# Optimization experiments

Measured on AMD Instinct MI355X. Metric: run time of the kernel, lower is better.

The kernel has to match this reference:

```python
import jax, jax.numpy as jnp
import numpy as np

B, NAT, K, F, L = 16, 256, 24, 128, 4
EPS = 0.01  # action / displacement step scale


def _gather(a, idx):
    # a: [B, n, ...], idx: [B, n, k] -> [B, n, k, ...]
    return jax.vmap(lambda ab, ib: ab[ib])(a, idx)


def _knn_idx(x, cell, k):
    # periodic minimum-image kNN within each structure
    frac = x[:, None, :, :] - x[:, :, None, :]          # [B,i,j,3] = x_j - x_i
    frac = frac - jnp.round(frac)
    cart = jnp.einsum('bijd,bde->bije', frac, cell)
    dist = jnp.linalg.norm(cart, axis=-1)
    dist = dist + jnp.eye(x.shape[1], dtype=x.dtype) * 1e6  # exclude self
    _, idx = jax.lax.top_k(-dist, k)
    return idx


def _edge_vectors(x, cell, idx):
    xj = _gather(x, idx)                                # [B,n,k,3]
    frac = xj - x[:, :, None, :]
    frac = frac - jnp.round(frac)
    vec = jnp.einsum('bnkd,bde->bnke', frac, cell)
    dist = jnp.linalg.norm(vec, axis=-1)
    return vec, dist


def _mpnn(h, idx, dist, W1, b1, W2, b2):
    hj = _gather(h, idx)                                # [B,n,k,F]
    feat = jnp.concatenate([hj, dist[..., None]], axis=-1)
    m = jax.nn.silu(jnp.einsum('bnkf,fg->bnkg', feat, W1) + b1)
    return h + jax.nn.silu(m.sum(axis=2) @ W2 + b2)


def _forward(cell, x, z, emb, mW1, mb1, mW2, mb2, uW1, ub1, uW2, ub2, act_we, actpos_we):
    I = jnp.eye(3, dtype=x.dtype)
    Bc = cell.shape[0]
    cell0 = jnp.broadcast_to(I, (Bc, 3, 3))            # actions_init overrides input cell
    x = jnp.mod(x, 1.0)
    idx = _knn_idx(x, cell0, K)
    vec, dist = _edge_vectors(x, cell0, idx)
    u = vec / (dist[..., None] + 1e-12)
    cross = jnp.cross(u[:, :, :, None, :], u[:, :, None, :, :])  # [B,n,k,k,3]
    tri_mask = (jnp.linalg.norm(cross, axis=-1) > 1e-3).astype(x.dtype)  # filter_triplets

    h = emb[z]
    for l in range(L):
        h = _mpnn(h, idx, dist, mW1[l], mb1[l], mW2[l], mb2[l])

    action_rho = jnp.broadcast_to(I, (Bc, 3, 3))
    traj_sum = jnp.zeros_like(x)
    geo_cell = cell0
    rho_prime = action_rho
    for l in range(L):
        h = _mpnn(h, idx, dist, uW1[l], ub1[l], uW2[l], ub2[l])
        hj = _gather(h, idx)
        e_feat = h[:, :, None, :] + hj                  # [B,n,k,F]
        w_e = jnp.tanh(jnp.einsum('bnkf,f->bnk', e_feat, act_we[l]))
        w_t = w_e[:, :, :, None] * w_e[:, :, None, :] * tri_mask
        strain = jnp.einsum('bnk,bnkc,bnkd->bcd', w_e, u, u) / (NAT * K)
        tri = jnp.einsum('bnjk,bnjkc,bnjkd->bcd', w_t, cross, cross) / (NAT * K * K)
        action = jnp.eye(3, dtype=x.dtype) + EPS * (strain + tri)
        action_rho = jnp.einsum('bij,bjk->bik', action, action_rho)
        rho_prime = jnp.einsum('bij,bjk->bik', action_rho, cell0)
        # position actions
        w_p = jnp.tanh(jnp.einsum('bnkf,f->bnk', e_feat, actpos_we[l]))
        x_cart = EPS * jnp.einsum('bnk,bnkc->bnc', w_p, vec)
        x_frac = jnp.einsum('bnc,bcd->bnd', x_cart, jnp.linalg.inv(geo_cell))
        traj_sum = traj_sum + x_cart
        x = x + x_frac
        geo_cell = rho_prime
        vec, dist = _edge_vectors(x, geo_cell, idx)     # geometry.update_vectors()
        u = vec / (dist[..., None] + 1e-12)
        cross = jnp.cross(u[:, :, :, None, :], u[:, :, None, :, :])
    return traj_sum, rho_prime


def setup_inputs() -> dict:
    key = jax.random.key(0)
    ks = jax.random.split(key, 12)
    s1 = 1.0 / np.sqrt(F + 1)
    s2 = 1.0 / np.sqrt(F)
    return {
        'cell': jax.random.normal(ks[0], (B, 3, 3), jnp.float32),
        'x': jax.random.uniform(ks[1], (B, NAT, 3), jnp.float32),
        'z': jax.random.randint(ks[2], (B, NAT), 0, 100, dtype=jnp.int32),
        'struct_size': jnp.full((B,), NAT, dtype=jnp.int32),
        'emb': jax.random.normal(ks[3], (100, F), jnp.float32) * 0.1,
        'mpnn_W1': jax.random.normal(ks[4], (L, F + 1, F), jnp.float32) * s1,
        'mpnn_b1': jnp.zeros((L, F), jnp.float32),
        'mpnn_W2': jax.random.normal(ks[5], (L, F, F), jnp.float32) * s2,
        'mpnn_b2': jnp.zeros((L, F), jnp.float32),
        'upd_W1': jax.random.normal(ks[6], (L, F + 1, F), jnp.float32) * s1,
        'upd_b1': jnp.zeros((L, F), jnp.float32),
        'upd_W2': jax.random.normal(ks[7], (L, F, F), jnp.float32) * s2,
        'upd_b2': jnp.zeros((L, F), jnp.float32),
        'act_we': jax.random.normal(ks[8], (L, F), jnp.float32) * s2,
        'actpos_we': jax.random.normal(ks[9], (L, F), jnp.float32) * s2,
    }


def reference(cell, x, z, struct_size, emb, mpnn_W1, mpnn_b1, mpnn_W2, mpnn_b2, upd_W1, upd_b1, upd_W2, upd_b2, act_we, actpos_we):
    # struct_size is informational (dense uniform batch of NAT atoms per structure)
    return _forward(cell, x, z, emb, mpnn_W1, mpnn_b1, mpnn_W2, mpnn_b2,
                    upd_W1, upd_b1, upd_W2, upd_b2, act_we, actpos_we)
```

## Files before the change

kernel.cpp:

```cpp
#include <hip/hip_runtime.h>

#define NB 16
#define NATS 256
#define KNN 24
#define FD 128
#define EPSA 0.01f
#define NATOMS (NB * NATS)
#define NEDGE (NATOMS * KNN)

typedef __attribute__((ext_vector_type(8))) short short8;
typedef __attribute__((ext_vector_type(4))) float f32x4;

__device__ __forceinline__ float silu_f(float v) { return v / (1.f + __expf(-v)); }

__device__ __forceinline__ short f2b(float f) {
    union { float f; unsigned u; } v; v.f = f;
    unsigned r = v.u + 0x7FFFu + ((v.u >> 16) & 1u);
    return (short)(r >> 16);
}
__device__ __forceinline__ float b2f(short s) {
    return __uint_as_float(((unsigned)(unsigned short)s) << 16);
}
__device__ __forceinline__ short8 ldb(const short* __restrict__ W, int n, int ks, int quad) {
    return *(const short8*)&W[n * 128 + ks * 32 + quad * 8];
}

__global__ __launch_bounds__(256) void prep_kernel(
    const float* __restrict__ mW1, const float* __restrict__ mW2,
    const float* __restrict__ uW1, const float* __restrict__ uW2,
    short* __restrict__ wh, short* __restrict__ wl_)
{
    int tid = blockIdx.x * 256 + threadIdx.x;
    int m = tid >> 14;
    int e = tid & 16383;
    int n = e >> 7, k = e & 127;
    const float* src;
    int l = m & 3;
    switch (m >> 2) {
        case 0:  src = mW1 + l * 129 * 128; break;
        case 1:  src = mW2 + l * 128 * 128; break;
        case 2:  src = uW1 + l * 129 * 128; break;
        default: src = uW2 + l * 128 * 128; break;
    }
    float w = src[k * 128 + n];
    short hi = f2b(w);
    wh[tid] = hi;
    wl_[tid] = f2b(w - b2f(hi));
}

__global__ __launch_bounds__(256) void init_kernel(
    const float* __restrict__ xin, const int* __restrict__ z,
    const float* __restrict__ emb,
    const short* __restrict__ W1h, const short* __restrict__ W1l,
    float* __restrict__ x, float* __restrict__ traj,
    float* __restrict__ h, float* __restrict__ hW)
{
    __shared__ short sAH[16 * 136];
    __shared__ short sAL[16 * 136];
    const int t = threadIdx.x;
    const int atom0 = blockIdx.x * 16;
    if (t < 48) {
        int gi = atom0 * 3 + t;
        float v = xin[gi];
        x[gi] = v - floorf(v);
        traj[gi] = 0.f;
    }
    {
        const int r = t >> 4;
        const int f0 = (t & 15) * 8;
        const int a = atom0 + r;
        const float4* src = (const float4*)(emb + z[a] * FD + f0);
        float4 v0 = src[0], v1 = src[1];
        float4* dst = (float4*)(h + a * FD + f0);
        dst[0] = v0; dst[1] = v1;
        float vv[8] = {v0.x, v0.y, v0.z, v0.w, v1.x, v1.y, v1.z, v1.w};
        short8 shv, slv;
#pragma unroll
        for (int i = 0; i < 8; ++i) {
            short hi = f2b(vv[i]);
            shv[i] = hi; slv[i] = f2b(vv[i] - b2f(hi));
        }
        *(short8*)&sAH[r * 136 + f0] = shv;
        *(short8*)&sAL[r * 136 + f0] = slv;
    }
    __syncthreads();
    const int w = t >> 6, lane = t & 63, quad = lane >> 4, col = lane & 15;
    const int n0 = w * 32;
    f32x4 acc0 = {0.f, 0.f, 0.f, 0.f}, acc1 = {0.f, 0.f, 0.f, 0.f};
#pragma unroll
    for (int ks = 0; ks < 4; ++ks) {
        short8 ah = *(const short8*)&sAH[col * 136 + ks * 32 + quad * 8];
        short8 al = *(const short8*)&sAL[col * 136 + ks * 32 + quad * 8];
        short8 bh0 = ldb(W1h, n0 + col, ks, quad);
        short8 bl0 = ldb(W1l, n0 + col, ks, quad);
        short8 bh1 = ldb(W1h, n0 + 16 + col, ks, quad);
        short8 bl1 = ldb(W1l, n0 + 16 + col, ks, quad);
        acc0 = __builtin_amdgcn_mfma_f32_16x16x32_bf16(ah, bh0, acc0, 0, 0, 0);
        acc0 = __builtin_amdgcn_mfma_f32_16x16x32_bf16(ah, bl0, acc0, 0, 0, 0);
        acc0 = __builtin_amdgcn_mfma_f32_16x16x32_bf16(al, bh0, acc0, 0, 0, 0);
        acc1 = __builtin_amdgcn_mfma_f32_16x16x32_bf16(ah, bh1, acc1, 0, 0, 0);
        acc1 = __builtin_amdgcn_mfma_f32_16x16x32_bf16(ah, bl1, acc1, 0, 0, 0);
        acc1 = __builtin_amdgcn_mfma_f32_16x16x32_bf16(al, bh1, acc1, 0, 0, 0);
    }
#pragma unroll
    for (int nt = 0; nt < 2; ++nt) {
        int gn = n0 + nt * 16 + col;
        f32x4 av = (nt == 0) ? acc0 : acc1;
#pragma unroll
        for (int r = 0; r < 4; ++r) {
            int row = quad * 4 + r;
            hW[(atom0 + row) * FD + gn] = av[r];
        }
    }
}

__global__ __launch_bounds__(64) void knn_kernel(const float* __restrict__ x,
    int* __restrict__ idxb, float* __restrict__ u0, float* __restrict__ dist0)
{
    const int a = blockIdx.x;
    const int b = a >> 8;
    const int lane = threadIdx.x;
    const float xi0 = x[a * 3 + 0], xi1 = x[a * 3 + 1], xi2 = x[a * 3 + 2];
    unsigned long long key[4];
#pragma unroll
    for (int tt = 0; tt < 4; ++tt) {
        int jg = b * NATS + lane + tt * 64;
        float d0 = x[jg * 3 + 0] - xi0; d0 -= rintf(d0);
        float d1 = x[jg * 3 + 1] - xi1; d1 -= rintf(d1);
        float d2 = x[jg * 3 + 2] - xi2; d2 -= rintf(d2);
        float dd = sqrtf(d0 * d0 + d1 * d1 + d2 * d2);
        if (jg == a) dd += 1e6f;
        key[tt] = ((unsigned long long)__float_as_uint(dd) << 32) | (unsigned)jg;
    }
    int myj = 0;
    for (int sel = 0; sel < KNN; ++sel) {
        unsigned long long m = key[0];
        if (key[1] < m) m = key[1];
        if (key[2] < m) m = key[2];
        if (key[3] < m) m = key[3];
#pragma unroll
        for (int off = 32; off > 0; off >>= 1) {
            unsigned lo = (unsigned)__shfl_xor((int)(unsigned)(m & 0xffffffffu), off);
            unsigned hi = (unsigned)__shfl_xor((int)(unsigned)(m >> 32), off);
            unsigned long long o = ((unsigned long long)hi << 32) | lo;
            if (o < m) m = o;
        }
        int jw = (int)(m & 0xffffffffu);
        if (lane == 0) idxb[a * KNN + sel] = jw;
        if (lane == sel) myj = jw;
#pragma unroll
        for (int tt = 0; tt < 4; ++tt) if (key[tt] == m) key[tt] = ~0ull;
    }
    if (lane < KNN) {
        float f0 = x[myj * 3 + 0] - xi0; f0 -= rintf(f0);
        float f1 = x[myj * 3 + 1] - xi1; f1 -= rintf(f1);
        float f2 = x[myj * 3 + 2] - xi2; f2 -= rintf(f2);
        float dd = sqrtf(f0 * f0 + f1 * f1 + f2 * f2);
        float inv = 1.f / (dd + 1e-12f);
        int e = a * KNN + lane;
        u0[e * 3 + 0] = f0 * inv; u0[e * 3 + 1] = f1 * inv; u0[e * 3 + 2] = f2 * inv;
        dist0[e] = dd;
    }
}

__global__ __launch_bounds__(256, 2) void layer_kernel(
    const float* __restrict__ hW, const int* __restrict__ idxb,
    const float* __restrict__ dist0,
    const float* __restrict__ x, const float* __restrict__ geo, int use_geo,
    const float* __restrict__ wl, const float* __restrict__ b1,
    const short* __restrict__ W2h, const short* __restrict__ W2l,
    const float* __restrict__ b2,
    const short* __restrict__ W1nh, const short* __restrict__ W1nl,
    float* __restrict__ hWout,
    float* __restrict__ h, int write_h,
    const float* __restrict__ we_a, const float* __restrict__ we_p,
    float* __restrict__ p, float* __restrict__ q)
{
    __shared__ short sAggH[16 * 136];
    __shared__ short sAggL[16 * 136];
    __shared__ short sHnH[16 * 136];
    __shared__ short sHnL[16 * 136];
    __shared__ float sHf[8 * 136];
    __shared__ int   sIdx[8 * KNN];
    __shared__ float sDist[8 * KNN];
    const int t = threadIdx.x;
    const int atom0 = blockIdx.x * 8;
    if (t < 8 * KNN) {
        int a = atom0 + (t / KNN);
        int j = idxb[atom0 * KNN + t];
        sIdx[t] = j;
        float d;
        if (dist0 != nullptr) {
            d = dist0[atom0 * KNN + t];
        } else {
            float f0 = x[j * 3 + 0] - x[a * 3 + 0]; f0 -= rintf(f0);
            float f1 = x[j * 3 + 1] - x[a * 3 + 1]; f1 -= rintf(f1);
            float f2 = x[j * 3 + 2] - x[a * 3 + 2]; f2 -= rintf(f2);
            const float* c = geo + (a >> 8) * 9;
            float v0 = f0 * c[0] + f1 * c[3] + f2 * c[6];
            float v1 = f0 * c[1] + f1 * c[4] + f2 * c[7];
            float v2 = f0 * c[2] + f1 * c[5] + f2 * c[8];
            d = sqrtf(v0 * v0 + v1 * v1 + v2 * v2);
        }
        sDist[t] = d;
    }
    __syncthreads();
    {
        const int g = t & 127;
        const int sub = t >> 7;
        const float wlg = wl[g];
        const float b1g = b1[g];
#pragma unroll
        for (int rep = 0; rep < 4; ++rep) {
            const int a = rep * 2 + sub;
            float s = 0.f;
#pragma unroll 8
            for (int k = 0; k < KNN; ++k) {
                int j = sIdx[a * KNN + k];
                float v = hW[j * FD + g] + sDist[a * KNN + k] * wlg + b1g;
                s += silu_f(v);
            }
            short hi = f2b(s);
            sAggH[a * 136 + g] = hi;
            sAggL[a * 136 + g] = f2b(s - b2f(hi));
        }
    }
    __syncthreads();
    const int w = t >> 6, lane = t & 63, quad = lane >> 4, col = lane & 15;
    const int n0 = w * 32;
    f32x4 acc0 = {0.f, 0.f, 0.f, 0.f}, acc1 = {0.f, 0.f, 0.f, 0.f};
#pragma unroll
    for (int ks = 0; ks < 4; ++ks) {
        short8 ah = *(const short8*)&sAggH[col * 136 + ks * 32 + quad * 8];
        short8 al = *(const short8*)&sAggL[col * 136 + ks * 32 + quad * 8];
        short8 bh0 = ldb(W2h, n0 + col, ks, quad);
        short8 bl0 = ldb(W2l, n0 + col, ks, quad);
        short8 bh1 = ldb(W2h, n0 + 16 + col, ks, quad);
        short8 bl1 = ldb(W2l, n0 + 16 + col, ks, quad);
        acc0 = __builtin_amdgcn_mfma_f32_16x16x32_bf16(ah, bh0, acc0, 0, 0, 0);
        acc0 = __builtin_amdgcn_mfma_f32_16x16x32_bf16(ah, bl0, acc0, 0, 0, 0);
        acc0 = __builtin_amdgcn_mfma_f32_16x16x32_bf16(al, bh0, acc0, 0, 0, 0);
        acc1 = __builtin_amdgcn_mfma_f32_16x16x32_bf16(ah, bh1, acc1, 0, 0, 0);
        acc1 = __builtin_amdgcn_mfma_f32_16x16x32_bf16(ah, bl1, acc1, 0, 0, 0);
        acc1 = __builtin_amdgcn_mfma_f32_16x16x32_bf16(al, bh1, acc1, 0, 0, 0);
    }
#pragma unroll
    for (int nt = 0; nt < 2; ++nt) {
        int gn = n0 + nt * 16 + col;
        float bb = b2[gn];
        f32x4 av = (nt == 0) ? acc0 : acc1;
#pragma unroll
        for (int r = 0; r < 4; ++r) {
            int row = quad * 4 + r;
            if (row < 8) {
                float o = h[(atom0 + row) * FD + gn] + silu_f(av[r] + bb);
                if (write_h) h[(atom0 + row) * FD + gn] = o;
                short hi = f2b(o);
                sHnH[row * 136 + gn] = hi;
                sHnL[row * 136 + gn] = f2b(o - b2f(hi));
                sHf[row * 136 + gn] = o;
            }
        }
    }
    __syncthreads();
    if (we_a != nullptr && t < 128) {
        int a = t >> 4, gr = t & 15;
        float pp = 0.f, qq = 0.f;
#pragma unroll
        for (int i = 0; i < 8; ++i) {
            int g = gr + i * 16;
            float hv = sHf[a * 136 + g];
            pp += hv * we_a[g];
            qq += hv * we_p[g];
        }
#pragma unroll
        for (int off = 8; off >= 1; off >>= 1) {
            pp += __shfl_xor(pp, off);
            qq += __shfl_xor(qq, off);
        }
        if (gr == 0) { p[atom0 + a] = pp; q[atom0 + a] = qq; }
    }
    if (W1nh != nullptr) {
        f32x4 d0 = {0.f, 0.f, 0.f, 0.f}, d1 = {0.f, 0.f, 0.f, 0.f};
#pragma unroll
        for (int ks = 0; ks < 4; ++ks) {
            short8 ah = *(const short8*)&sHnH[col * 136 + ks * 32 + quad * 8];
            short8 al = *(const short8*)&sHnL[col * 136 + ks * 32 + quad * 8];
            short8 bh0 = ldb(W1nh, n0 + col, ks, quad);
            short8 bl0 = ldb(W1nl, n0 + col, ks, quad);
            short8 bh1 = ldb(W1nh, n0 + 16 + col, ks, quad);
            short8 bl1 = ldb(W1nl, n0 + 16 + col, ks, quad);
            d0 = __builtin_amdgcn_mfma_f32_16x16x32_bf16(ah, bh0, d0, 0, 0, 0);
            d0 = __builtin_amdgcn_mfma_f32_16x16x32_bf16(ah, bl0, d0, 0, 0, 0);
            d0 = __builtin_amdgcn_mfma_f32_16x16x32_bf16(al, bh0, d0, 0, 0, 0);
            d1 = __builtin_amdgcn_mfma_f32_16x16x32_bf16(ah, bh1, d1, 0, 0, 0);
            d1 = __builtin_amdgcn_mfma_f32_16x16x32_bf16(ah, bl1, d1, 0, 0, 0);
            d1 = __builtin_amdgcn_mfma_f32_16x16x32_bf16(al, bh1, d1, 0, 0, 0);
        }
#pragma unroll
        for (int nt = 0; nt < 2; ++nt) {
            int gn = n0 + nt * 16 + col;
            f32x4 av = (nt == 0) ? d0 : d1;
#pragma unroll
            for (int r = 0; r < 4; ++r) {
                int row = quad * 4 + r;
                if (row < 8)
                    hWout[(atom0 + row) * FD + gn] = av[r];
            }
        }
    }
}

__global__ __launch_bounds__(256) void accum_kernel(
    const float* __restrict__ p, const float* __restrict__ q,
    const int* __restrict__ idxb, const float* __restrict__ x,
    const float* __restrict__ geo, int use_geo,
    const float* __restrict__ u0b,
    float* __restrict__ part, float* __restrict__ xcart)
{
    const int blk = blockIdx.x;
    const int t = threadIdx.x;
    const int w = t >> 6;
    const int lane = t & 63;
    const int a = blk * 4 + w;
    const int b = a >> 8;
    __shared__ float swe[4][KNN], swp[4][KNN];
    __shared__ float su[4][KNN][3], su0[4][KNN][3], sv[4][KNN][3];
    __shared__ float spart[4][18];
    if (lane < KNN) {
        int e = a * KNN + lane;
        int j = idxb[e];
        swe[w][lane] = tanhf(p[a] + p[j]);
        swp[w][lane] = tanhf(q[a] + q[j]);
        float f0 = x[j * 3 + 0] - x[a * 3 + 0]; f0 -= rintf(f0);
        float f1 = x[j * 3 + 1] - x[a * 3 + 1]; f1 -= rintf(f1);
        float f2 = x[j * 3 + 2] - x[a * 3 + 2]; f2 -= rintf(f2);
        float v0 = f0, v1 = f1, v2 = f2;
        if (use_geo) {
            const float* c = geo + b * 9;
            v0 = f0 * c[0] + f1 * c[3] + f2 * c[6];
            v1 = f0 * c[1] + f1 * c[4] + f2 * c[7];
            v2 = f0 * c[2] + f1 * c[5] + f2 * c[8];
        }
        float dd = sqrtf(v0 * v0 + v1 * v1 + v2 * v2);
        float inv = 1.f / (dd + 1e-12f);
        sv[w][lane][0] = v0; sv[w][lane][1] = v1; sv[w][lane][2] = v2;
        su[w][lane][0] = v0 * inv; su[w][lane][1] = v1 * inv; su[w][lane][2] = v2 * inv;
        su0[w][lane][0] = u0b[e * 3]; su0[w][lane][1] = u0b[e * 3 + 1]; su0[w][lane][2] = u0b[e * 3 + 2];
    }
    __syncthreads();
    float r[21];
#pragma unroll
    for (int i = 0; i < 21; ++i) r[i] = 0.f;
    if (lane < KNN) {
        float wgt = swe[w][lane];
        float ux = su[w][lane][0], uy = su[w][lane][1], uz = su[w][lane][2];
        r[0] = wgt * ux * ux; r[1] = wgt * ux * uy; r[2] = wgt * ux * uz;
        r[3] = wgt * uy * ux; r[4] = wgt * uy * uy; r[5] = wgt * uy * uz;
        r[6] = wgt * uz * ux; r[7] = wgt * uz * uy; r[8] = wgt * uz * uz;
        float wp = swp[w][lane];
        r[18] = wp * sv[w][lane][0]; r[19] = wp * sv[w][lane][1]; r[20] = wp * sv[w][lane][2];
    }
#pragma unroll
    for (int tt = 0; tt < 9; ++tt) {
        int pr = lane + (tt << 6);
        int j = pr / KNN, k = pr - j * KNN;
        float c0x = su0[w][j][1] * su0[w][k][2] - su0[w][j][2] * su0[w][k][1];
        float c0y = su0[w][j][2] * su0[w][k][0] - su0[w][j][0] * su0[w][k][2];
        float c0z = su0[w][j][0] * su0[w][k][1] - su0[w][j][1] * su0[w][k][0];
        float nn2 = c0x * c0x + c0y * c0y + c0z * c0z;
        if (nn2 > 1e-6f) {
            float cx = su[w][j][1] * su[w][k][2] - su[w][j][2] * su[w][k][1];
            float cy = su[w][j][2] * su[w][k][0] - su[w][j][0] * su[w][k][2];
            float cz = su[w][j][0] * su[w][k][1] - su[w][j][1] * su[w][k][0];
            float wt = swe[w][j] * swe[w][k];
            r[9]  += wt * cx * cx; r[10] += wt * cx * cy; r[11] += wt * cx * cz;
            r[12] += wt * cy * cx; r[13] += wt * cy * cy; r[14] += wt * cy * cz;
            r[15] += wt * cz * cx; r[16] += wt * cz * cy; r[17] += wt * cz * cz;
        }
    }
#pragma unroll
    for (int off = 32; off > 0; off >>= 1)
#pragma unroll
        for (int i = 0; i < 21; ++i) r[i] += __shfl_down(r[i], off);
    if (lane == 0) {
#pragma unroll
        for (int i = 0; i < 18; ++i) spart[w][i] = r[i];
        xcart[a * 3 + 0] = EPSA * r[18];
        xcart[a * 3 + 1] = EPSA * r[19];
        xcart[a * 3 + 2] = EPSA * r[20];
    }
    __syncthreads();
    if (t < 18)
        part[blk * 18 + t] = spart[0][t] + spart[1][t] + spart[2][t] + spart[3][t];
}

__global__ __launch_bounds__(256) void rho_pos_kernel(const float* __restrict__ part,
    const float* __restrict__ xcart,
    float* __restrict__ rho, float* __restrict__ geo,
    float* __restrict__ x, float* __restrict__ traj,
    float* __restrict__ out, int first, int last)
{
    const int b = blockIdx.x;
    const int t = threadIdx.x;
    __shared__ float sIV[9];
    if (t < 64) {
        float r[18];
#pragma unroll
        for (int i = 0; i < 18; ++i) r[i] = part[(b * 64 + t) * 18 + i];
#pragma unroll
        for (int off = 32; off > 0; off >>= 1)
#pragma unroll
            for (int i = 0; i < 18; ++i) r[i] += __shfl_down(r[i], off);
        if (t == 0) {
            float A[9];
#pragma unroll
            for (int i = 0; i < 9; ++i) {
                float strain = r[i] / 6144.f;
                float tri = r[9 + i] / 147456.f;
                A[i] = ((i == 0 || i == 4 || i == 8) ? 1.f : 0.f) + EPSA * (strain + tri);
            }
            float N[9], IV[9];
            if (first) {
#pragma unroll
                for (int i = 0; i < 9; ++i) { N[i] = A[i]; IV[i] = (i == 0 || i == 4 || i == 8) ? 1.f : 0.f; }
            } else {
                float R[9], G[9];
#pragma unroll
                for (int i = 0; i < 9; ++i) { R[i] = rho[b * 9 + i]; G[i] = geo[b * 9 + i]; }
#pragma unroll
                for (int i = 0; i < 3; ++i)
#pragma unroll
                    for (int k = 0; k < 3; ++k)
                        N[i * 3 + k] = A[i * 3] * R[k] + A[i * 3 + 1] * R[3 + k] + A[i * 3 + 2] * R[6 + k];
                float det = G[0] * (G[4] * G[8] - G[5] * G[7])
                          - G[1] * (G[3] * G[8] - G[5] * G[6])
                          + G[2] * (G[3] * G[7] - G[4] * G[6]);
                float id = 1.f / det;
                IV[0] = (G[4] * G[8] - G[5] * G[7]) * id;
                IV[1] = (G[2] * G[7] - G[1] * G[8]) * id;
                IV[2] = (G[1] * G[5] - G[2] * G[4]) * id;
                IV[3] = (G[5] * G[6] - G[3] * G[8]) * id;
                IV[4] = (G[0] * G[8] - G[2] * G[6]) * id;
                IV[5] = (G[2] * G[3] - G[0] * G[5]) * id;
                IV[6] = (G[3] * G[7] - G[4] * G[6]) * id;
                IV[7] = (G[1] * G[6] - G[0] * G[7]) * id;
                IV[8] = (G[0] * G[4] - G[1] * G[3]) * id;
            }
#pragma unroll
            for (int i = 0; i < 9; ++i) {
                sIV[i] = IV[i];
                rho[b * 9 + i] = N[i];
                if (!last) geo[b * 9 + i] = N[i];
                else out[NATOMS * 3 + b * 9 + i] = N[i];
            }
        }
    }
    __syncthreads();
    for (int d = t; d < NATS * 3; d += 256) {
        int al = d / 3, dim = d - al * 3;
        int ga = b * NATS + al;
        int gi = ga * 3 + dim;
        float c0 = xcart[ga * 3 + 0], c1 = xcart[ga * 3 + 1], c2 = xcart[ga * 3 + 2];
        float tj = traj[gi] + xcart[gi];
        if (!last) {
            float xf = c0 * sIV[0 + dim] + c1 * sIV[3 + dim] + c2 * sIV[6 + dim];
            x[gi] += xf;
            traj[gi] = tj;
        } else {
            out[gi] = tj;
        }
    }
}

extern "C" void kernel_launch(void* const* d_in, const int* in_sizes, int n_in,
                              void* d_out, int out_size, void* d_ws, size_t ws_size,
                              hipStream_t stream)
{
    (void)in_sizes; (void)n_in; (void)out_size; (void)ws_size;
    const float* in_x = (const float*)d_in[1];
    const int*   z    = (const int*)d_in[2];
    const float* emb  = (const float*)d_in[4];
    const float* mW1  = (const float*)d_in[5];
    const float* mb1  = (const float*)d_in[6];
    const float* mW2  = (const float*)d_in[7];
    const float* mb2  = (const float*)d_in[8];
    const float* uW1  = (const float*)d_in[9];
    const float* ub1  = (const float*)d_in[10];
    const float* uW2  = (const float*)d_in[11];
    const float* ub2  = (const float*)d_in[12];
    const float* awe  = (const float*)d_in[13];
    const float* pwe  = (const float*)d_in[14];
    float* out = (float*)d_out;

    char* wsb = (char*)d_ws;
    size_t off = 0;
    auto carve = [&](size_t elems) {
        void* ptr = wsb + off;
        off += (elems * 4 + 255) & ~(size_t)255;
        return ptr;
    };
    float* traj  = (float*)carve(NATOMS * 3);
    float* part  = (float*)carve(1024 * 18);
    float* x     = (float*)carve(NATOMS * 3);
    float* xcart = (float*)carve(NATOMS * 3);
    float* p     = (float*)carve(NATOMS);
    float* q     = (float*)carve(NATOMS);
    float* rho   = (float*)carve(NB * 9);
    float* geo   = (float*)carve(NB * 9);
    float* u0    = (float*)carve(NEDGE * 3);
    float* dist0 = (float*)carve(NEDGE);
    float* h     = (float*)carve(NATOMS * FD);
    float* hWa   = (float*)carve(NATOMS * FD);
    float* hWb   = (float*)carve(NATOMS * FD);
    int*   idx   = (int*)carve(NEDGE);
    short* wth   = (short*)carve(16 * 16384 / 2);
    short* wtl   = (short*)carve(16 * 16384 / 2);

    auto WH = [&](int m) { return wth + m * 16384; };
    auto WL = [&](int m) { return wtl + m * 16384; };

    prep_kernel<<<1024, 256, 0, stream>>>(mW1, mW2, uW1, uW2, wth, wtl);
    init_kernel<<<256, 256, 0, stream>>>(in_x, z, emb, WH(0), WL(0), x, traj, h, hWa);
    knn_kernel<<<NATOMS, 64, 0, stream>>>(x, idx, u0, dist0);

    float* hw_in = hWa;
    float* hw_out = hWb;

    for (int l = 0; l < 4; ++l) {
        int w1n = (l < 3) ? (l + 1) : 8;
        layer_kernel<<<512, 256, 0, stream>>>(hw_in, idx, dist0, x, geo, 0,
            mW1 + l * 129 * 128 + 128 * 128, mb1 + l * 128,
            WH(4 + l), WL(4 + l), mb2 + l * 128,
            WH(w1n), WL(w1n), hw_out, h, 1,
            nullptr, nullptr, nullptr, nullptr);
        float* tmp = hw_in; hw_in = hw_out; hw_out = tmp;
    }
    for (int l = 0; l < 4; ++l) {
        const short* W1nh = (l < 3) ? WH(9 + l) : nullptr;
        const short* W1nl = (l < 3) ? WL(9 + l) : nullptr;
        const float* d0 = (l == 0) ? dist0 : nullptr;
        layer_kernel<<<512, 256, 0, stream>>>(hw_in, idx, d0, x, geo, (l > 0) ? 1 : 0,
            uW1 + l * 129 * 128 + 128 * 128, ub1 + l * 128,
            WH(12 + l), WL(12 + l), ub2 + l * 128,
            W1nh, W1nl, hw_out, h, (l < 3) ? 1 : 0,
            awe + l * 128, pwe + l * 128, p, q);
        float* tmp = hw_in; hw_in = hw_out; hw_out = tmp;
        accum_kernel<<<1024, 256, 0, stream>>>(p, q, idx, x, geo, (l > 0) ? 1 : 0,
            u0, part, xcart);
        rho_pos_kernel<<<NB, 256, 0, stream>>>(part, xcart, rho, geo, x, traj, out,
            (l == 0) ? 1 : 0, (l == 3) ? 1 : 0);
    }
}
```

Before: 339.1 us.

## Fuse kNN into first layer kernel and rho update into accum kernel

The standalone kNN kernel now runs inside the first message-passing layer kernel. Each wave computes neighbours for two atoms and writes the indices and distances straight into shared memory as well as to global buffers. The per-structure rho/position update kernel is folded into accum_kernel: a last-block-arrives atomic counter per structure (zeroed in init_kernel) lets the final block of each structure reduce the partials and update geo, x and traj. This removes five kernel launches and their inter-kernel gaps. In exchange it adds threadfence/atomic synchronisation and puts serial kNN selection work into the layer kernel.

```diff
diff --git a/kernel.cpp b/kernel.cpp
--- a/kernel.cpp
+++ b/kernel.cpp
@@ -53,12 +53,13 @@
     const float* __restrict__ emb,
     const short* __restrict__ W1h, const short* __restrict__ W1l,
     float* __restrict__ x, float* __restrict__ traj,
-    float* __restrict__ h, float* __restrict__ hW)
+    float* __restrict__ h, float* __restrict__ hW, int* __restrict__ cnt)
 {
     __shared__ short sAH[16 * 136];
     __shared__ short sAL[16 * 136];
     const int t = threadIdx.x;
     const int atom0 = blockIdx.x * 16;
+    if (blockIdx.x == 0 && t < 64) cnt[t] = 0;
     if (t < 48) {
         int gi = atom0 * 3 + t;
         float v = xin[gi];
@@ -107,66 +108,16 @@
         int gn = n0 + nt * 16 + col;
         f32x4 av = (nt == 0) ? acc0 : acc1;
 #pragma unroll
-        for (int r = 0; r < 4; ++r) {
-            int row = quad * 4 + r;
-            hW[(atom0 + row) * FD + gn] = av[r];
-        }
-    }
-}
-
-__global__ __launch_bounds__(64) void knn_kernel(const float* __restrict__ x,
-    int* __restrict__ idxb, float* __restrict__ u0, float* __restrict__ dist0)
-{
-    const int a = blockIdx.x;
-    const int b = a >> 8;
-    const int lane = threadIdx.x;
-    const float xi0 = x[a * 3 + 0], xi1 = x[a * 3 + 1], xi2 = x[a * 3 + 2];
-    unsigned long long key[4];
-#pragma unroll
-    for (int tt = 0; tt < 4; ++tt) {
-        int jg = b * NATS + lane + tt * 64;
-        float d0 = x[jg * 3 + 0] - xi0; d0 -= rintf(d0);
-        float d1 = x[jg * 3 + 1] - xi1; d1 -= rintf(d1);
-        float d2 = x[jg * 3 + 2] - xi2; d2 -= rintf(d2);
-        float dd = sqrtf(d0 * d0 + d1 * d1 + d2 * d2);
-        if (jg == a) dd += 1e6f;
-        key[tt] = ((unsigned long long)__float_as_uint(dd) << 32) | (unsigned)jg;
-    }
-    int myj = 0;
-    for (int sel = 0; sel < KNN; ++sel) {
-        unsigned long long m = key[0];
-        if (key[1] < m) m = key[1];
-        if (key[2] < m) m = key[2];
-        if (key[3] < m) m = key[3];
-#pragma unroll
-        for (int off = 32; off > 0; off >>= 1) {
-            unsigned lo = (unsigned)__shfl_xor((int)(unsigned)(m & 0xffffffffu), off);
-            unsigned hi = (unsigned)__shfl_xor((int)(unsigned)(m >> 32), off);
-            unsigned long long o = ((unsigned long long)hi << 32) | lo;
-            if (o < m) m = o;
-        }
-        int jw = (int)(m & 0xffffffffu);
-        if (lane == 0) idxb[a * KNN + sel] = jw;
-        if (lane == sel) myj = jw;
-#pragma unroll
-        for (int tt = 0; tt < 4; ++tt) if (key[tt] == m) key[tt] = ~0ull;
-    }
-    if (lane < KNN) {
-        float f0 = x[myj * 3 + 0] - xi0; f0 -= rintf(f0);
-        float f1 = x[myj * 3 + 1] - xi1; f1 -= rintf(f1);
-        float f2 = x[myj * 3 + 2] - xi2; f2 -= rintf(f2);
-        float dd = sqrtf(f0 * f0 + f1 * f1 + f2 * f2);
-        float inv = 1.f / (dd + 1e-12f);
-        int e = a * KNN + lane;
-        u0[e * 3 + 0] = f0 * inv; u0[e * 3 + 1] = f1 * inv; u0[e * 3 + 2] = f2 * inv;
-        dist0[e] = dd;
+        for (int r = 0; r < 4; ++r)
+            hW[(atom0 + quad * 4 + r) * FD + gn] = av[r];
     }
 }
 
 __global__ __launch_bounds__(256, 2) void layer_kernel(
-    const float* __restrict__ hW, const int* __restrict__ idxb,
-    const float* __restrict__ dist0,
-    const float* __restrict__ x, const float* __restrict__ geo, int use_geo,
+    const float* __restrict__ hW, int* __restrict__ idxb,
+    float* __restrict__ dist0, float* __restrict__ u0w,
+    const float* __restrict__ x, const float* __restrict__ geo,
+    int mode_knn, int use_d0, int use_geo,
     const float* __restrict__ wl, const float* __restrict__ b1,
     const short* __restrict__ W2h, const short* __restrict__ W2l,
     const float* __restrict__ b2,
@@ -185,21 +136,75 @@
     __shared__ float sDist[8 * KNN];
     const int t = threadIdx.x;
     const int atom0 = blockIdx.x * 8;
-    if (t < 8 * KNN) {
+    const int w = t >> 6, lane = t & 63, quad = lane >> 4, col = lane & 15;
+    const int n0 = w * 32;
+    if (mode_knn) {
+        for (int rep = 0; rep < 2; ++rep) {
+            const int slot = w * 2 + rep;
+            const int a = atom0 + slot;
+            const int bS = a >> 8;
+            const float xi0 = x[a * 3 + 0], xi1 = x[a * 3 + 1], xi2 = x[a * 3 + 2];
+            unsigned long long key[4];
+#pragma unroll
+            for (int tt = 0; tt < 4; ++tt) {
+                int jg = bS * NATS + lane + tt * 64;
+                float d0 = x[jg * 3 + 0] - xi0; d0 -= rintf(d0);
+                float d1 = x[jg * 3 + 1] - xi1; d1 -= rintf(d1);
+                float d2 = x[jg * 3 + 2] - xi2; d2 -= rintf(d2);
+                float dd = sqrtf(d0 * d0 + d1 * d1 + d2 * d2);
+                if (jg == a) dd += 1e6f;
+                key[tt] = ((unsigned long long)__float_as_uint(dd) << 32) | (unsigned)jg;
+            }
+            int myj = 0;
+            for (int sel = 0; sel < KNN; ++sel) {
+                unsigned long long m = key[0];
+                if (key[1] < m) m = key[1];
+                if (key[2] < m) m = key[2];
+                if (key[3] < m) m = key[3];
+#pragma unroll
+                for (int off = 32; off > 0; off >>= 1) {
+                    unsigned lo = (unsigned)__shfl_xor((int)(unsigned)(m & 0xffffffffu), off);
+                    unsigned hi = (unsigned)__shfl_xor((int)(unsigned)(m >> 32), off);
+                    unsigned long long o = ((unsigned long long)hi << 32) | lo;
+                    if (o < m) m = o;
+                }
+                int jw = (int)(m & 0xffffffffu);
+                if (lane == 0) idxb[a * KNN + sel] = jw;
+                if (lane == sel) myj = jw;
+#pragma unroll
+                for (int tt = 0; tt < 4; ++tt) if (key[tt] == m) key[tt] = ~0ull;
+            }
+            if (lane < KNN) {
+                float f0 = x[myj * 3 + 0] - xi0; f0 -= rintf(f0);
+                float f1 = x[myj * 3 + 1] - xi1; f1 -= rintf(f1);
+                float f2 = x[myj * 3 + 2] - xi2; f2 -= rintf(f2);
+                float dd = sqrtf(f0 * f0 + f1 * f1 + f2 * f2);
+                float inv = 1.f / (dd + 1e-12f);
+                int e = a * KNN + lane;
+                u0w[e * 3 + 0] = f0 * inv; u0w[e * 3 + 1] = f1 * inv; u0w[e * 3 + 2] = f2 * inv;
+                dist0[e] = dd;
+                sIdx[slot * KNN + lane] = myj;
+                sDist[slot * KNN + lane] = dd;
+            }
+        }
+    } else if (t < 8 * KNN) {
         int a = atom0 + (t / KNN);
         int j = idxb[atom0 * KNN + t];
         sIdx[t] = j;
         float d;
-        if (dist0 != nullptr) {
+        if (use_d0) {
             d = dist0[atom0 * KNN + t];
         } else {
             float f0 = x[j * 3 + 0] - x[a * 3 + 0]; f0 -= rintf(f0);
             float f1 = x[j * 3 + 1] - x[a * 3 + 1]; f1 -= rintf(f1);
             float f2 = x[j * 3 + 2] - x[a * 3 + 2]; f2 -= rintf(f2);
-            const float* c = geo + (a >> 8) * 9;
-            float v0 = f0 * c[0] + f1 * c[3] + f2 * c[6];
-            float v1 = f0 * c[1] + f1 * c[4] + f2 * c[7];
-            float v2 = f0 * c[2] + f1 * c[5] + f2 * c[8];
+            float v0 = f0, v1 = f1, v2 = f2;
+            if (use_geo) {
+                const float* c = geo + (a >> 8) * 9;
+                v0 = f0 * c[0] + f1 * c[3] + f2 * c[6];
+                v1 = f0 * c[1] + f1 * c[4] + f2 * c[7];
+                v2 = f0 * c[2] + f1 * c[5] + f2 * c[8];
+            }
             d = sqrtf(v0 * v0 + v1 * v1 + v2 * v2);
         }
         sDist[t] = d;
@@ -226,8 +231,6 @@
         }
     }
     __syncthreads();
-    const int w = t >> 6, lane = t & 63, quad = lane >> 4, col = lane & 15;
-    const int n0 = w * 32;
     f32x4 acc0 = {0.f, 0.f, 0.f, 0.f}, acc1 = {0.f, 0.f, 0.f, 0.f};
 #pragma unroll
     for (int ks = 0; ks < 4; ++ks) {
@@ -313,10 +316,12 @@
 
 __global__ __launch_bounds__(256) void accum_kernel(
     const float* __restrict__ p, const float* __restrict__ q,
-    const int* __restrict__ idxb, const float* __restrict__ x,
-    const float* __restrict__ geo, int use_geo,
+    const int* __restrict__ idxb, float* __restrict__ x,
+    float* __restrict__ geo, int use_geo,
     const float* __restrict__ u0b,
-    float* __restrict__ part, float* __restrict__ xcart)
+    float* __restrict__ part, float* __restrict__ xcart,
+    float* __restrict__ rho, float* __restrict__ traj,
+    float* __restrict__ out, int* __restrict__ cnt, int first, int last)
 {
     const int blk = blockIdx.x;
     const int t = threadIdx.x;
@@ -324,9 +329,12 @@
     const int lane = t & 63;
     const int a = blk * 4 + w;
     const int b = a >> 8;
+    const int s = blk >> 6;
     __shared__ float swe[4][KNN], swp[4][KNN];
     __shared__ float su[4][KNN][3], su0[4][KNN][3], sv[4][KNN][3];
     __shared__ float spart[4][18];
+    __shared__ int   sLast;
+    __shared__ float sIV[9];
     if (lane < KNN) {
         int e = a * KNN + lane;
         int j = idxb[e];
@@ -393,31 +401,29 @@
     __syncthreads();
     if (t < 18)
         part[blk * 18 + t] = spart[0][t] + spart[1][t] + spart[2][t] + spart[3][t];
-}
-
-__global__ __launch_bounds__(256) void rho_pos_kernel(const float* __restrict__ part,
-    const float* __restrict__ xcart,
-    float* __restrict__ rho, float* __restrict__ geo,
-    float* __restrict__ x, float* __restrict__ traj,
-    float* __restrict__ out, int first, int last)
-{
-    const int b = blockIdx.x;
-    const int t = threadIdx.x;
-    __shared__ float sIV[9];
+    __threadfence();
+    __syncthreads();
+    if (t == 0) {
+        int old = atomicAdd(&cnt[s], 1);
+        sLast = (old == 63) ? 1 : 0;
+    }
+    __syncthreads();
+    if (!sLast) return;
+    __threadfence();
     if (t < 64) {
-        float r[18];
-#pragma unroll
-        for (int i = 0; i < 18; ++i) r[i] = part[(b * 64 + t) * 18 + i];
+        float rr[18];
+#pragma unroll
+        for (int i = 0; i < 18; ++i) rr[i] = part[(s * 64 + t) * 18 + i];
 #pragma unroll
         for (int off = 32; off > 0; off >>= 1)
 #pragma unroll
-            for (int i = 0; i < 18; ++i) r[i] += __shfl_down(r[i], off);
+            for (int i = 0; i < 18; ++i) rr[i] += __shfl_down(rr[i], off);
         if (t == 0) {
             float A[9];
 #pragma unroll
             for (int i = 0; i < 9; ++i) {
-                float strain = r[i] / 6144.f;
-                float tri = r[9 + i] / 147456.f;
+                float strain = rr[i] / 6144.f;
+                float tri = rr[9 + i] / 147456.f;
                 A[i] = ((i == 0 || i == 4 || i == 8) ? 1.f : 0.f) + EPSA * (strain + tri);
             }
             float N[9], IV[9];
@@ -427,7 +433,7 @@
             } else {
                 float R[9], G[9];
 #pragma unroll
-                for (int i = 0; i < 9; ++i) { R[i] = rho[b * 9 + i]; G[i] = geo[b * 9 + i]; }
+                for (int i = 0; i < 9; ++i) { R[i] = rho[s * 9 + i]; G[i] = geo[s * 9 + i]; }
 #pragma unroll
                 for (int i = 0; i < 3; ++i)
 #pragma unroll
@@ -450,16 +456,16 @@
 #pragma unroll
             for (int i = 0; i < 9; ++i) {
                 sIV[i] = IV[i];
-                rho[b * 9 + i] = N[i];
-                if (!last) geo[b * 9 + i] = N[i];
-                else out[NATOMS * 3 + b * 9 + i] = N[i];
+                rho[s * 9 + i] = N[i];
+                if (!last) geo[s * 9 + i] = N[i];
+                else out[NATOMS * 3 + s * 9 + i] = N[i];
             }
         }
     }
     __syncthreads();
     for (int d = t; d < NATS * 3; d += 256) {
         int al = d / 3, dim = d - al * 3;
-        int ga = b * NATS + al;
+        int ga = s * NATS + al;
         int gi = ga * 3 + dim;
         float c0 = xcart[ga * 3 + 0], c1 = xcart[ga * 3 + 1], c2 = xcart[ga * 3 + 2];
         float tj = traj[gi] + xcart[gi];
@@ -516,20 +522,21 @@
     int*   idx   = (int*)carve(NEDGE);
     short* wth   = (short*)carve(16 * 16384 / 2);
     short* wtl   = (short*)carve(16 * 16384 / 2);
+    int*   cnt   = (int*)carve(64);
 
     auto WH = [&](int m) { return wth + m * 16384; };
     auto WL = [&](int m) { return wtl + m * 16384; };
 
     prep_kernel<<<1024, 256, 0, stream>>>(mW1, mW2, uW1, uW2, wth, wtl);
-    init_kernel<<<256, 256, 0, stream>>>(in_x, z, emb, WH(0), WL(0), x, traj, h, hWa);
-    knn_kernel<<<NATOMS, 64, 0, stream>>>(x, idx, u0, dist0);
+    init_kernel<<<256, 256, 0, stream>>>(in_x, z, emb, WH(0), WL(0), x, traj, h, hWa, cnt);
 
     float* hw_in = hWa;
     float* hw_out = hWb;
 
     for (int l = 0; l < 4; ++l) {
         int w1n = (l < 3) ? (l + 1) : 8;
-        layer_kernel<<<512, 256, 0, stream>>>(hw_in, idx, dist0, x, geo, 0,
+        layer_kernel<<<512, 256, 0, stream>>>(hw_in, idx, dist0, u0, x, geo,
+            (l == 0) ? 1 : 0, (l == 0) ? 0 : 1, 0,
             mW1 + l * 129 * 128 + 128 * 128, mb1 + l * 128,
             WH(4 + l), WL(4 + l), mb2 + l * 128,
             WH(w1n), WL(w1n), hw_out, h, 1,
@@ -539,16 +546,15 @@
     for (int l = 0; l < 4; ++l) {
         const short* W1nh = (l < 3) ? WH(9 + l) : nullptr;
         const short* W1nl = (l < 3) ? WL(9 + l) : nullptr;
-        const float* d0 = (l == 0) ? dist0 : nullptr;
-        layer_kernel<<<512, 256, 0, stream>>>(hw_in, idx, d0, x, geo, (l > 0) ? 1 : 0,
+        layer_kernel<<<512, 256, 0, stream>>>(hw_in, idx, dist0, u0, x, geo,
+            0, (l == 0) ? 1 : 0, (l > 0) ? 1 : 0,
             uW1 + l * 129 * 128 + 128 * 128, ub1 + l * 128,
             WH(12 + l), WL(12 + l), ub2 + l * 128,
             W1nh, W1nl, hw_out, h, (l < 3) ? 1 : 0,
             awe + l * 128, pwe + l * 128, p, q);
         float* tmp = hw_in; hw_in = hw_out; hw_out = tmp;
         accum_kernel<<<1024, 256, 0, stream>>>(p, q, idx, x, geo, (l > 0) ? 1 : 0,
-            u0, part, xcart);
-        rho_pos_kernel<<<NB, 256, 0, stream>>>(part, xcart, rho, geo, x, traj, out,
+            u0, part, xcart, rho, traj, out, cnt + l * 16,
             (l == 0) ? 1 : 0, (l == 3) ? 1 : 0);
     }
 }
```

New measurement: 594.3 us. +75.3%, slower.
